# Kernel tuning notes

Hardware: AMD Instinct MI355X
Metric: run time of the kernel (lower is better)

## Reference

```python
import jax, jax.numpy as jnp
import numpy as np

KERNEL_SIZE = 16
STRIDE = 8
NEG = -1.0e9


def setup_inputs() -> dict:
    key = jax.random.key(0)
    k1, k2, k3, k4, k5 = jax.random.split(key, 5)
    B, C, L = 8, 512, 4096
    x = jax.random.normal(k1, (B, C, L), dtype=jnp.float32)
    mask = jax.random.randint(k2, (B, L), 0, 2).astype(bool)
    W = jax.random.normal(k3, (C, C), dtype=jnp.float32) * 0.02
    b = jax.random.normal(k4, (C,), dtype=jnp.float32) * 0.02
    v = jax.random.normal(k5, (C,), dtype=jnp.float32) * 0.02
    return {"x": x, "mask": mask, "W": W, "b": b, "v": v}


def reference(x, mask, W, b, v):
    # x: [B, C, L], mask: [B, L] (True = masked out)
    B, C, L = x.shape
    win, step = KERNEL_SIZE, STRIDE
    L_pool = 1 + (L - win) // step
    # per-token projection (identical across windows since proj is per-token)
    h = jnp.tanh(jnp.einsum('bcl,dc->bld', x, W) + b)      # [B, L, C]
    s = jnp.einsum('bld,d->bl', h, v)                       # [B, L]
    idx = jnp.arange(L_pool)[:, None] * step + jnp.arange(win)[None, :]
    sw = s[:, idx]
    mw = mask[:, idx]
    sw = jnp.where(mw, NEG, sw)
    w = jax.nn.softmax(sw, axis=-1)
    w = jnp.where(mw, 0.0, w)
    norm = jnp.clip(jnp.sum(w, axis=-1, keepdims=True), 1e-6, None)
    w = w / norm
    xw = x[:, :, idx]
    return jnp.einsum('bcpw,bpw->bcp', xw, w)               # [B, C, L_pool]
```

## Files before the change

kernel.cpp:

```cpp
#include <hip/hip_runtime.h>
#include <hip/hip_bf16.h>
#include <cmath>

#define Bsz 8
#define Csz 512
#define Lsz 4096
#define LPOOL 511
#define NEGV -1000000000.0f

typedef __attribute__((ext_vector_type(8))) short short8;
typedef __attribute__((ext_vector_type(4))) float float4v;

__device__ __forceinline__ float bf2f(short u) {
  unsigned int x = ((unsigned int)(unsigned short)u) << 16;
  return __builtin_bit_cast(float, x);
}

__device__ __forceinline__ float ftanh(float x) {
  float e = __expf(2.0f * x);
  return 1.0f - 2.0f * __builtin_amdgcn_rcpf(e + 1.0f);
}

__device__ __forceinline__ void gl_lds16(const __hip_bfloat16* g, void* l) {
  __builtin_amdgcn_global_load_lds(
      (const __attribute__((address_space(1))) unsigned int*)g,
      (__attribute__((address_space(3))) unsigned int*)l, 16, 0, 0);
}

__global__ __launch_bounds__(256) void prep(const unsigned char* __restrict__ mb,
    int* __restrict__ flag, const float* __restrict__ W,
    __hip_bfloat16* __restrict__ Wts) {
  const int tid = threadIdx.x;
  const int pb = blockIdx.x;
  if (pb == 0) {
    __shared__ int sf;
    if (tid == 0) sf = 0;
    __syncthreads();
    int f = 0;
    for (int i = tid; i < 4096; i += 256)
      if ((i & 3) && mb[i]) f = 1;
    if (f) atomicOr(&sf, 1);
    __syncthreads();
    if (tid == 0) *flag = sf;
  } else {
    int tg = (pb - 1) * 256 + tid;
    int d = tg >> 6, cg = tg & 63;
    float4 w0 = *(const float4*)(W + (size_t)d * 512 + cg * 8);
    float4 w1 = *(const float4*)(W + (size_t)d * 512 + cg * 8 + 4);
    __hip_bfloat16 hb[8];
    hb[0] = __float2bfloat16(w0.x); hb[1] = __float2bfloat16(w0.y);
    hb[2] = __float2bfloat16(w0.z); hb[3] = __float2bfloat16(w0.w);
    hb[4] = __float2bfloat16(w1.x); hb[5] = __float2bfloat16(w1.y);
    hb[6] = __float2bfloat16(w1.z); hb[7] = __float2bfloat16(w1.w);
    int nt = d >> 7, row = d & 127, ks = cg >> 2, seg = cg & 3;
    *(short8*)(Wts + (((size_t)nt * 16 + ks) * 512 + seg * 128 + row) * 8) = *(short8*)hb;
  }
}

__global__ __launch_bounds__(256, 1) void gemm_fused(
    const float* __restrict__ x, const __hip_bfloat16* __restrict__ Wts,
    const float* __restrict__ bias, const float* __restrict__ v,
    float* __restrict__ s, __hip_bfloat16* __restrict__ xbf) {
  __shared__ short8 sA[8192];
  __shared__ short8 sB[2][512];
  __shared__ float  sX[4][16][33];

  const int tid = threadIdx.x;
  const int lane = tid & 63, wave = tid >> 6;
  const int mt = blockIdx.x;
  const int b = mt >> 5;
  const int l0 = (mt & 31) << 7;

  {
    const int r = lane >> 2;
    const int q = lane & 3;
    const size_t rowbase = (((size_t)(b * Csz + r)) << 12) + (size_t)l0 + wave * 32 + q * 8;
    const float* xg = x + rowbase;
    const int ll = lane & 31, kseg = lane >> 5;

    float4 a0 = *(const float4*)(xg);
    float4 a1 = *(const float4*)(xg + 4);
    float4 b0 = *(const float4*)(xg + (1u << 16));
    float4 b1 = *(const float4*)(xg + (1u << 16) + 4);
    float4 c0 = a0, c1 = a1;

    for (int cc = 0; cc < 32; ++cc) {
      if (cc < 30) {
        const float* xn = xg + ((size_t)(cc + 2) << 16);
        c0 = *(const float4*)(xn);
        c1 = *(const float4*)(xn + 4);
      }
      __hip_bfloat16 hb[8];
      hb[0] = __float2bfloat16(a0.x); hb[1] = __float2bfloat16(a0.y);
      hb[2] = __float2bfloat16(a0.z); hb[3] = __float2bfloat16(a0.w);
      hb[4] = __float2bfloat16(a1.x); hb[5] = __float2bfloat16(a1.y);
      hb[6] = __float2bfloat16(a1.z); hb[7] = __float2bfloat16(a1.w);
      *(short8*)(xbf + rowbase + ((size_t)cc << 16)) = *(short8*)hb;
      *(float4*)(&sX[wave][r][q * 8])     = a0;
      *(float4*)(&sX[wave][r][q * 8 + 4]) = a1;
      asm volatile("s_waitcnt lgkmcnt(0)" ::: "memory");
      __builtin_amdgcn_sched_barrier(0);
      float tv[8];
      #pragma unroll
      for (int j = 0; j < 8; ++j) tv[j] = sX[wave][kseg * 8 + j][ll];
      __hip_bfloat16 ab[8];
      #pragma unroll
      for (int j = 0; j < 8; ++j) ab[j] = __float2bfloat16(tv[j]);
      const int k0 = cc * 16 + kseg * 8;
      const int ks = k0 >> 5, seg = (k0 >> 3) & 3;
      sA[(ks * 4 + seg) * 128 + wave * 32 + ll] = *(short8*)ab;
      asm volatile("s_waitcnt lgkmcnt(0)" ::: "memory");
      __builtin_amdgcn_sched_barrier(0);
      a0 = b0; a1 = b1; b0 = c0; b1 = c1;
    }
  }

  const int lr = lane & 15, quad = lane >> 4;
  float bl[4][8], vl[4][8];
  #pragma unroll
  for (int nt = 0; nt < 4; ++nt)
    #pragma unroll
    for (int nf = 0; nf < 8; ++nf) {
      int n = nt * 128 + nf * 16 + lr;
      bl[nt][nf] = bias[n];
      vl[nt][nf] = v[n];
    }

  {
    const __hip_bfloat16* gb = Wts + (size_t)(wave * 64 + lane) * 8;
    gl_lds16(gb,        &sB[0][wave * 64]);
    gl_lds16(gb + 2048, &sB[0][256 + wave * 64]);
  }
  __syncthreads();

  float4v acc[2][8];
  float sp[2][4];
  #pragma unroll
  for (int mf = 0; mf < 2; ++mf) {
    #pragma unroll
    for (int nf = 0; nf < 8; ++nf) acc[mf][nf] = (float4v)0.f;
    #pragma unroll
    for (int reg = 0; reg < 4; ++reg) sp[mf][reg] = 0.f;
  }

  #pragma unroll
  for (int nt = 0; nt < 4; ++nt) {
    #pragma unroll 2
    for (int ks = 0; ks < 16; ++ks) {
      const int idx = nt * 16 + ks;
      const int cur = idx & 1;
      if (idx < 63) {
        const __hip_bfloat16* gb =
            Wts + ((size_t)(idx + 1) << 12) + (size_t)(wave * 64 + lane) * 8;
        gl_lds16(gb,        &sB[cur ^ 1][wave * 64]);
        gl_lds16(gb + 2048, &sB[cur ^ 1][256 + wave * 64]);
        asm volatile("s_waitcnt vmcnt(2)" ::: "memory");
      } else {
        asm volatile("s_waitcnt vmcnt(0)" ::: "memory");
      }
      __builtin_amdgcn_sched_barrier(0);
      __builtin_amdgcn_s_barrier();
      short8 af[2], bfr[8];
      #pragma unroll
      for (int mf = 0; mf < 2; ++mf)
        af[mf] = sA[(ks * 4 + quad) * 128 + wave * 32 + mf * 16 + lr];
      #pragma unroll
      for (int nf = 0; nf < 8; ++nf)
        bfr[nf] = sB[cur][quad * 128 + nf * 16 + lr];
      #pragma unroll
      for (int mf = 0; mf < 2; ++mf)
        #pragma unroll
        for (int nf = 0; nf < 8; ++nf)
          acc[mf][nf] = __builtin_amdgcn_mfma_f32_16x16x32_bf16(
              af[mf], bfr[nf], acc[mf][nf], 0, 0, 0);
      __builtin_amdgcn_s_barrier();
    }
    #pragma unroll
    for (int mf = 0; mf < 2; ++mf) {
      #pragma unroll
      for (int reg = 0; reg < 4; ++reg) {
        float pp = 0.f;
        #pragma unroll
        for (int nf = 0; nf < 8; ++nf)
          pp += ftanh(acc[mf][nf][reg] + bl[nt][nf]) * vl[nt][nf];
        sp[mf][reg] += pp;
      }
      #pragma unroll
      for (int nf = 0; nf < 8; ++nf) acc[mf][nf] = (float4v)0.f;
    }
  }

  #pragma unroll
  for (int mf = 0; mf < 2; ++mf)
    #pragma unroll
    for (int reg = 0; reg < 4; ++reg) {
      float pv = sp[mf][reg];
      pv += __shfl_xor(pv, 1, 16);
      pv += __shfl_xor(pv, 2, 16);
      pv += __shfl_xor(pv, 4, 16);
      pv += __shfl_xor(pv, 8, 16);
      if (lr == 0)
        s[mt * 128 + wave * 32 + mf * 16 + quad * 4 + reg] = pv;
    }
}

__global__ __launch_bounds__(256) void pool2(const __hip_bfloat16* __restrict__ xbf,
    const float* __restrict__ s, const void* __restrict__ mask,
    const int* __restrict__ flag, float* __restrict__ out) {
  __shared__ float wl[8][17];
  const int t = threadIdx.x;
  const int p0 = blockIdx.x * 8, b = blockIdx.y;
  if (t < 8 && p0 + t < LPOOL) {
    const int p = p0 + t;
    const bool u8 = (*flag != 0);
    const unsigned char* m8 = (const unsigned char*)mask;
    const int* m32 = (const int*)mask;
    const int base = b * Lsz + p * 8;
    float sv[16]; int mv[16];
    float mx = -3.4e38f;
    #pragma unroll
    for (int w = 0; w < 16; ++w) {
      int mk = u8 ? (int)m8[base + w] : m32[base + w];
      float val = mk ? NEGV : s[base + w];
      sv[w] = val; mv[w] = mk;
      mx = fmaxf(mx, val);
    }
    float sum = 0.f;
    #pragma unroll
    for (int w = 0; w < 16; ++w) { sv[w] = expf(sv[w] - mx); sum += sv[w]; }
    float inv = 1.0f / sum;
    float norm = 0.f;
    #pragma unroll
    for (int w = 0; w < 16; ++w) { sv[w] = mv[w] ? 0.f : sv[w] * inv; norm += sv[w]; }
    norm = fmaxf(norm, 1e-6f);
    float rn = 1.0f / norm;
    #pragma unroll
    for (int w = 0; w < 16; ++w) wl[t][w] = sv[w] * rn;
  }
  __syncthreads();
  const int ci = t >> 3, pi = t & 7;
  const int p = p0 + pi;
  if (p >= LPOOL) return;
  float wr[16];
  #pragma unroll
  for (int w = 0; w < 16; ++w) wr[w] = wl[pi][w];
  #pragma unroll 4
  for (int it = 0; it < 16; ++it) {
    int c = it * 32 + ci;
    const __hip_bfloat16* xp = xbf + ((size_t)b * Csz + c) * Lsz + 8 * p;
    short8 lo = *(const short8*)xp;
    short8 hi = *(const short8*)(xp + 8);
    float acc = 0.f;
    #pragma unroll
    for (int j = 0; j < 8; ++j)
      acc += bf2f(lo[j]) * wr[j] + bf2f(hi[j]) * wr[8 + j];
    out[((size_t)b * Csz + c) * LPOOL + p] = acc;
  }
}

__global__ void detect_mask(const unsigned char* __restrict__ mb, int* __restrict__ flag) {
  __shared__ int sf;
  int t = threadIdx.x;
  if (t == 0) sf = 0;
  __syncthreads();
  int f = 0;
  for (int i = t; i < 4096; i += 256)
    if ((i & 3) && mb[i]) f = 1;
  if (f) atomicOr(&sf, 1);
  __syncthreads();
  if (t == 0) *flag = sf;
}

__global__ __launch_bounds__(256) void gemm_s_f32(const float* __restrict__ x,
    const float* __restrict__ W, const float* __restrict__ bias,
    const float* __restrict__ v, float* __restrict__ s_out) {
  __shared__ float sA[32][64];
  __shared__ float sB[32][68];
  __shared__ float s_acc[64];
  const int tid = threadIdx.x;
  const int b = blockIdx.y;
  const int l0 = blockIdx.x * 64;
  if (tid < 64) s_acc[tid] = 0.0f;
  const int tx = tid & 15;
  const int ty = tid >> 4;
  const float* xb = x + ((size_t)b * Csz) * Lsz + l0;
  for (int d0 = 0; d0 < Csz; d0 += 64) {
    float acc[4][4] = {{0.f}};
    for (int c0 = 0; c0 < Csz; c0 += 32) {
      __syncthreads();
      #pragma unroll
      for (int it = 0; it < 8; ++it) {
        int idx = tid + it * 256;
        int kc = idx >> 6, ml = idx & 63;
        sA[kc][ml] = xb[(size_t)(c0 + kc) * Lsz + ml];
      }
      #pragma unroll
      for (int it = 0; it < 8; ++it) {
        int idx = tid + it * 256;
        int kc = idx & 31, dj = idx >> 5;
        sB[kc][dj] = W[(size_t)(d0 + dj) * Csz + c0 + kc];
      }
      __syncthreads();
      #pragma unroll
      for (int kc = 0; kc < 32; ++kc) {
        float4 a  = *(const float4*)(&sA[kc][tx << 2]);
        float4 w4 = *(const float4*)(&sB[kc][ty << 2]);
        acc[0][0] += a.x * w4.x; acc[0][1] += a.x * w4.y; acc[0][2] += a.x * w4.z; acc[0][3] += a.x * w4.w;
        acc[1][0] += a.y * w4.x; acc[1][1] += a.y * w4.y; acc[1][2] += a.y * w4.z; acc[1][3] += a.y * w4.w;
        acc[2][0] += a.z * w4.x; acc[2][1] += a.z * w4.y; acc[2][2] += a.z * w4.z; acc[2][3] += a.z * w4.w;
        acc[3][0] += a.w * w4.x; acc[3][1] += a.w * w4.y; acc[3][2] += a.w * w4.z; acc[3][3] += a.w * w4.w;
      }
    }
    float part[4] = {0.f, 0.f, 0.f, 0.f};
    #pragma unroll
    for (int j = 0; j < 4; ++j) {
      int d = d0 + (ty << 2) + j;
      float bj = bias[d], vj = v[d];
      #pragma unroll
      for (int i = 0; i < 4; ++i)
        part[i] += tanhf(acc[i][j] + bj) * vj;
    }
    #pragma unroll
    for (int i = 0; i < 4; ++i)
      atomicAdd(&s_acc[(tx << 2) + i], part[i]);
  }
  __syncthreads();
  if (tid < 64) s_out[(size_t)b * Lsz + l0 + tid] = s_acc[tid];
}

__global__ void win_weights(const float* __restrict__ s, const void* __restrict__ mask,
                            const int* __restrict__ flag, float* __restrict__ wgt) {
  int t = blockIdx.x * blockDim.x + threadIdx.x;
  if (t >= Bsz * LPOOL) return;
  int b = t / LPOOL, p = t - b * LPOOL;
  const bool u8 = (*flag != 0);
  const unsigned char* m8 = (const unsigned char*)mask;
  const int* m32 = (const int*)mask;
  float sv[16]; int mv[16];
  float mx = -3.4e38f;
  int base = b * Lsz + p * 8;
  #pragma unroll
  for (int w = 0; w < 16; ++w) {
    int mk = u8 ? (int)m8[base + w] : m32[base + w];
    float val = mk ? NEGV : s[base + w];
    sv[w] = val; mv[w] = mk;
    mx = fmaxf(mx, val);
  }
  float sum = 0.f;
  #pragma unroll
  for (int w = 0; w < 16; ++w) { sv[w] = expf(sv[w] - mx); sum += sv[w]; }
  float inv = 1.0f / sum;
  float norm = 0.f;
  #pragma unroll
  for (int w = 0; w < 16; ++w) { sv[w] = mv[w] ? 0.f : sv[w] * inv; norm += sv[w]; }
  norm = fmaxf(norm, 1e-6f);
  float rn = 1.0f / norm;
  #pragma unroll
  for (int w = 0; w < 16; ++w) wgt[t * 16 + w] = sv[w] * rn;
}

__global__ __launch_bounds__(256) void pool_out(const float* __restrict__ x,
    const float* __restrict__ wgt, float* __restrict__ out) {
  __shared__ float xrow[Lsz];
  int bc = blockIdx.x;
  int c = bc & (Csz - 1);
  int b = bc >> 9;
  const float* xr = x + ((size_t)b * Csz + c) * Lsz;
  int tid = threadIdx.x;
  #pragma unroll
  for (int it = 0; it < 4; ++it) {
    int idx = (tid + it * 256) << 2;
    *(float4*)(&xrow[idx]) = *(const float4*)(&xr[idx]);
  }
  __syncthreads();
  const float* wb = wgt + (size_t)b * LPOOL * 16;
  float* ob = out + ((size_t)b * Csz + c) * LPOOL;
  for (int p = tid; p < LPOOL; p += 256) {
    const float4* wp = (const float4*)(wb + p * 16);
    const float4* xp = (const float4*)(&xrow[p * 8]);
    float acc = 0.f;
    #pragma unroll
    for (int q = 0; q < 4; ++q) {
      float4 wv = wp[q], xv = xp[q];
      acc += xv.x * wv.x + xv.y * wv.y + xv.z * wv.z + xv.w * wv.w;
    }
    ob[p] = acc;
  }
}

extern "C" void kernel_launch(void* const* d_in, const int* in_sizes, int n_in,
                              void* d_out, int out_size, void* d_ws, size_t ws_size,
                              hipStream_t stream) {
  const float* x    = (const float*)d_in[0];
  const void*  mask = d_in[1];
  const float* W    = (const float*)d_in[2];
  const float* bias = (const float*)d_in[3];
  const float* v    = (const float*)d_in[4];
  float* out = (float*)d_out;

  char* wsb = (char*)d_ws;
  int*   flag = (int*)wsb;
  float* s    = (float*)(wsb + 256);
  float* wgt  = (float*)(wsb + 131328);
  __hip_bfloat16* Wts = (__hip_bfloat16*)(wsb + 393216);
  __hip_bfloat16* xbf = (__hip_bfloat16*)(wsb + 917504);
  const size_t NEED = 917504 + 33554432;

  if (ws_size >= NEED) {
    prep<<<129, 256, 0, stream>>>((const unsigned char*)mask, flag, W, Wts);
    gemm_fused<<<256, 256, 0, stream>>>(x, Wts, bias, v, s, xbf);
    pool2<<<dim3(64, Bsz), 256, 0, stream>>>(xbf, s, mask, flag, out);
  } else {
    detect_mask<<<1, 256, 0, stream>>>((const unsigned char*)mask, flag);
    gemm_s_f32<<<dim3(Lsz / 64, Bsz), 256, 0, stream>>>(x, W, bias, v, s);
    win_weights<<<(Bsz * LPOOL + 255) / 256, 256, 0, stream>>>(s, mask, flag, wgt);
    pool_out<<<Bsz * Csz, 256, 0, stream>>>(x, wgt, out);
  }
}
```

Measured before the change: 169.9 us.

## Use 8 waves per block in fused GEMM, halving rows per wave

Doubles the gemm_fused block from 256 to 512 threads, so each wave handles 16 of the 128 rows instead of 32, with one M-fragment instead of two. Each thread loads one W tile chunk instead of two, and the transpose scratch aliases the W double buffer in a shared LDS pool to keep shared memory small. The goal is more waves per CU to hide global x loads and MFMA latency, with fewer accumulator registers per thread. The cost is that every wave now reads the full B tile from LDS for only half the MFMA work, and the larger block takes more barriers.

```diff
diff --git a/kernel.cpp b/kernel.cpp
--- a/kernel.cpp
+++ b/kernel.cpp
@@ -57,13 +57,12 @@
   }
 }
 
-__global__ __launch_bounds__(256, 1) void gemm_fused(
+__global__ __launch_bounds__(512, 2) void gemm_fused(
     const float* __restrict__ x, const __hip_bfloat16* __restrict__ Wts,
     const float* __restrict__ bias, const float* __restrict__ v,
     float* __restrict__ s, __hip_bfloat16* __restrict__ xbf) {
   __shared__ short8 sA[8192];
-  __shared__ short8 sB[2][512];
-  __shared__ float  sX[4][16][33];
+  __shared__ __align__(16) char sPool[17408];
 
   const int tid = threadIdx.x;
   const int lane = tid & 63, wave = tid >> 6;
@@ -72,21 +71,23 @@
   const int l0 = (mt & 31) << 7;
 
   {
-    const int r = lane >> 2;
-    const int q = lane & 3;
-    const size_t rowbase = (((size_t)(b * Csz + r)) << 12) + (size_t)l0 + wave * 32 + q * 8;
+    float* sXw = (float*)sPool + wave * 544;
+    const int r = lane >> 1;
+    const int q = lane & 1;
+    const size_t rowbase =
+        (((size_t)(b * Csz + r)) << 12) + (size_t)(l0 + wave * 16 + q * 8);
     const float* xg = x + rowbase;
-    const int ll = lane & 31, kseg = lane >> 5;
+    const int ll = lane & 15, kseg = lane >> 4;
 
     float4 a0 = *(const float4*)(xg);
     float4 a1 = *(const float4*)(xg + 4);
-    float4 b0 = *(const float4*)(xg + (1u << 16));
-    float4 b1 = *(const float4*)(xg + (1u << 16) + 4);
+    float4 b0 = *(const float4*)(xg + (1u << 17));
+    float4 b1 = *(const float4*)(xg + (1u << 17) + 4);
     float4 c0 = a0, c1 = a1;
 
-    for (int cc = 0; cc < 32; ++cc) {
-      if (cc < 30) {
-        const float* xn = xg + ((size_t)(cc + 2) << 16);
+    for (int cc = 0; cc < 16; ++cc) {
+      if (cc < 14) {
+        const float* xn = xg + ((size_t)(cc + 2) << 17);
         c0 = *(const float4*)(xn);
         c1 = *(const float4*)(xn + 4);
       }
@@ -95,20 +96,18 @@
       hb[2] = __float2bfloat16(a0.z); hb[3] = __float2bfloat16(a0.w);
       hb[4] = __float2bfloat16(a1.x); hb[5] = __float2bfloat16(a1.y);
       hb[6] = __float2bfloat16(a1.z); hb[7] = __float2bfloat16(a1.w);
-      *(short8*)(xbf + rowbase + ((size_t)cc << 16)) = *(short8*)hb;
-      *(float4*)(&sX[wave][r][q * 8])     = a0;
-      *(float4*)(&sX[wave][r][q * 8 + 4]) = a1;
+      *(short8*)(xbf + rowbase + ((size_t)cc << 17)) = *(short8*)hb;
+      *(float4*)(&sXw[r * 17 + q * 8])     = a0;
+      *(float4*)(&sXw[r * 17 + q * 8 + 4]) = a1;
       asm volatile("s_waitcnt lgkmcnt(0)" ::: "memory");
       __builtin_amdgcn_sched_barrier(0);
       float tv[8];
       #pragma unroll
-      for (int j = 0; j < 8; ++j) tv[j] = sX[wave][kseg * 8 + j][ll];
+      for (int j = 0; j < 8; ++j) tv[j] = sXw[(kseg * 8 + j) * 17 + ll];
       __hip_bfloat16 ab[8];
       #pragma unroll
       for (int j = 0; j < 8; ++j) ab[j] = __float2bfloat16(tv[j]);
-      const int k0 = cc * 16 + kseg * 8;
-      const int ks = k0 >> 5, seg = (k0 >> 3) & 3;
-      sA[(ks * 4 + seg) * 128 + wave * 32 + ll] = *(short8*)ab;
+      sA[(cc * 4 + kseg) * 128 + wave * 16 + ll] = *(short8*)ab;
       asm volatile("s_waitcnt lgkmcnt(0)" ::: "memory");
       __builtin_amdgcn_sched_barrier(0);
       a0 = b0; a1 = b1; b0 = c0; b1 = c1;
@@ -126,22 +125,17 @@
       vl[nt][nf] = v[n];
     }
 
-  {
-    const __hip_bfloat16* gb = Wts + (size_t)(wave * 64 + lane) * 8;
-    gl_lds16(gb,        &sB[0][wave * 64]);
-    gl_lds16(gb + 2048, &sB[0][256 + wave * 64]);
-  }
-  __syncthreads();
-
-  float4v acc[2][8];
-  float sp[2][4];
-  #pragma unroll
-  for (int mf = 0; mf < 2; ++mf) {
-    #pragma unroll
-    for (int nf = 0; nf < 8; ++nf) acc[mf][nf] = (float4v)0.f;
-    #pragma unroll
-    for (int reg = 0; reg < 4; ++reg) sp[mf][reg] = 0.f;
-  }
+  __syncthreads();
+  short8 (*sB)[512] = (short8 (*)[512])sPool;
+  gl_lds16(Wts + (size_t)(wave * 64 + lane) * 8, &sB[0][wave * 64]);
+  __syncthreads();
+
+  float4v acc[8];
+  float sp[4];
+  #pragma unroll
+  for (int nf = 0; nf < 8; ++nf) acc[nf] = (float4v)0.f;
+  #pragma unroll
+  for (int reg = 0; reg < 4; ++reg) sp[reg] = 0.f;
 
   #pragma unroll
   for (int nt = 0; nt < 4; ++nt) {
@@ -152,56 +146,45 @@
       if (idx < 63) {
         const __hip_bfloat16* gb =
             Wts + ((size_t)(idx + 1) << 12) + (size_t)(wave * 64 + lane) * 8;
-        gl_lds16(gb,        &sB[cur ^ 1][wave * 64]);
-        gl_lds16(gb + 2048, &sB[cur ^ 1][256 + wave * 64]);
-        asm volatile("s_waitcnt vmcnt(2)" ::: "memory");
+        gl_lds16(gb, &sB[cur ^ 1][wave * 64]);
+        asm volatile("s_waitcnt vmcnt(1)" ::: "memory");
       } else {
         asm volatile("s_waitcnt vmcnt(0)" ::: "memory");
       }
       __builtin_amdgcn_sched_barrier(0);
       __builtin_amdgcn_s_barrier();
-      short8 af[2], bfr[8];
-      #pragma unroll
-      for (int mf = 0; mf < 2; ++mf)
-        af[mf] = sA[(ks * 4 + quad) * 128 + wave * 32 + mf * 16 + lr];
+      short8 af = sA[(ks * 4 + quad) * 128 + wave * 16 + lr];
+      short8 bfr[8];
       #pragma unroll
       for (int nf = 0; nf < 8; ++nf)
         bfr[nf] = sB[cur][quad * 128 + nf * 16 + lr];
       #pragma unroll
-      for (int mf = 0; mf < 2; ++mf)
-        #pragma unroll
-        for (int nf = 0; nf < 8; ++nf)
-          acc[mf][nf] = __builtin_amdgcn_mfma_f32_16x16x32_bf16(
-              af[mf], bfr[nf], acc[mf][nf], 0, 0, 0);
+      for (int nf = 0; nf < 8; ++nf)
+        acc[nf] = __builtin_amdgcn_mfma_f32_16x16x32_bf16(af, bfr[nf], acc[nf], 0, 0, 0);
       __builtin_amdgcn_s_barrier();
     }
     #pragma unroll
-    for (int mf = 0; mf < 2; ++mf) {
-      #pragma unroll
-      for (int reg = 0; reg < 4; ++reg) {
-        float pp = 0.f;
-        #pragma unroll
-        for (int nf = 0; nf < 8; ++nf)
-          pp += ftanh(acc[mf][nf][reg] + bl[nt][nf]) * vl[nt][nf];
-        sp[mf][reg] += pp;
-      }
-      #pragma unroll
-      for (int nf = 0; nf < 8; ++nf) acc[mf][nf] = (float4v)0.f;
-    }
-  }
-
-  #pragma unroll
-  for (int mf = 0; mf < 2; ++mf)
-    #pragma unroll
     for (int reg = 0; reg < 4; ++reg) {
-      float pv = sp[mf][reg];
-      pv += __shfl_xor(pv, 1, 16);
-      pv += __shfl_xor(pv, 2, 16);
-      pv += __shfl_xor(pv, 4, 16);
-      pv += __shfl_xor(pv, 8, 16);
-      if (lr == 0)
-        s[mt * 128 + wave * 32 + mf * 16 + quad * 4 + reg] = pv;
-    }
+      float pp = 0.f;
+      #pragma unroll
+      for (int nf = 0; nf < 8; ++nf)
+        pp += ftanh(acc[nf][reg] + bl[nt][nf]) * vl[nt][nf];
+      sp[reg] += pp;
+    }
+    #pragma unroll
+    for (int nf = 0; nf < 8; ++nf) acc[nf] = (float4v)0.f;
+  }
+
+  #pragma unroll
+  for (int reg = 0; reg < 4; ++reg) {
+    float pv = sp[reg];
+    pv += __shfl_xor(pv, 1, 16);
+    pv += __shfl_xor(pv, 2, 16);
+    pv += __shfl_xor(pv, 4, 16);
+    pv += __shfl_xor(pv, 8, 16);
+    if (lr == 0)
+      s[mt * 128 + wave * 16 + quad * 4 + reg] = pv;
+  }
 }
 
 __global__ __launch_bounds__(256) void pool2(const __hip_bfloat16* __restrict__ xbf,
@@ -408,7 +391,7 @@
 
   if (ws_size >= NEED) {
     prep<<<129, 256, 0, stream>>>((const unsigned char*)mask, flag, W, Wts);
-    gemm_fused<<<256, 256, 0, stream>>>(x, Wts, bias, v, s, xbf);
+    gemm_fused<<<256, 512, 0, stream>>>(x, Wts, bias, v, s, xbf);
     pool2<<<dim3(64, Bsz), 256, 0, stream>>>(xbf, s, mask, flag, out);
   } else {
     detect_mask<<<1, 256, 0, stream>>>((const unsigned char*)mask, flag);
```

Measured after the change: 163.9 us. 3.5% less time.
